# Kernel optimization log

Measured on AMD Instinct MI355X. Metric: run time of the kernel, lower is better.

Reference implementation:

```python
import jax, jax.numpy as jnp
from jax import lax
import numpy as np


def _conv(x, w):
    # x: [B,Cin,H,W], w: [Cout,Cin,kh,kw] -> [B,Cout,H,W], SAME padding
    return lax.conv_general_dilated(x, w, (1, 1), 'SAME')


def setup_inputs() -> dict:
    key = jax.random.key(0)
    ks = jax.random.split(key, 16)
    B, Hh, W = 8, 256, 256
    inputs = jax.random.normal(ks[0], (B, Hh, W), jnp.float32)
    H0 = jax.random.normal(ks[1], (B, Hh, W), jnp.float32)
    C0 = jax.random.normal(ks[2], (B, 2, Hh, W), jnp.float32)
    # learned scalars: c2 ~ U(0,1), sf ~ N(0, 0.01) shifted away from 0 (it is a divisor)
    c2 = jax.random.uniform(ks[3], (1,), jnp.float32, 0.0, 1.0)
    sf = 0.01 * jax.random.normal(ks[4], (1,), jnp.float32) + 0.02
    # RedNet (assumed small conv encoder-decoder): 1->32->64->32->1, 3x3 SAME, ReLU
    w1 = 0.1 * jax.random.normal(ks[5], (32, 1, 3, 3), jnp.float32)
    b1 = jnp.zeros((32,), jnp.float32)
    w2 = 0.1 * jax.random.normal(ks[6], (64, 32, 3, 3), jnp.float32)
    b2 = jnp.zeros((64,), jnp.float32)
    w3 = 0.1 * jax.random.normal(ks[7], (32, 64, 3, 3), jnp.float32)
    b3 = jnp.zeros((32,), jnp.float32)
    w4 = 0.1 * jax.random.normal(ks[8], (1, 32, 3, 3), jnp.float32)
    b4 = jnp.zeros((1,), jnp.float32)
    return dict(inputs=inputs, H0=H0, C0=C0, c2=c2, sf=sf,
                w1=w1, b1=b1, w2=w2, b2=b2, w3=w3, b3=b3, w4=w4, b4=b4)


def reference(inputs, H0, C0, c2, sf, w1, b1, w2, b2, w3, b3, w4, b4):
    # Fixed 5-point Laplacian stencil (non-trainable in the original module)
    lap_k = jnp.array([[0., 1., 0.], [1., -4., 1.], [0., 1., 0.]],
                      dtype=inputs.dtype)[None, None]  # [1,1,3,3]

    # torch chain: C' = permute/matmul(Wcc^T)/permute + wcu*U
    #   reduces exactly to: C'[:,0] = inputs, C'[:,1] = C_old[:,0]
    C_new = jnp.stack([inputs, C0[:, 0]], axis=1)  # [B,2,H,W]

    V = inputs - H0  # [B,H,W]

    # H = whc . C' = 2*C'[:,0] - C'[:,1] = 2*inputs - C_old[:,0]
    lap = _conv(inputs[:, None], lap_k)[:, 0]  # [B,H,W]
    H = 2.0 * inputs - C0[:, 0] + c2 * lap

    # RedNet on scaled residual V
    h = (V / sf)[:, None]  # [B,1,H,W]
    h = jax.nn.relu(_conv(h, w1) + b1[None, :, None, None])
    h = jax.nn.relu(_conv(h, w2) + b2[None, :, None, None])
    h = jax.nn.relu(_conv(h, w3) + b3[None, :, None, None])
    V_hat = (_conv(h, w4) + b4[None, :, None, None])[:, 0] * sf  # [B,H,W]

    outputs = H + V_hat
    return (outputs, H, C_new, V, V_hat)
```

## Files before the change

kernel.cpp:

```cpp
#include <hip/hip_runtime.h>

#define PLANE 65536
#define WIDTH 256
#define PADW 258
#define PADPLANE 66564

typedef __bf16 v8bf __attribute__((ext_vector_type(8)));
typedef float  v4f  __attribute__((ext_vector_type(4)));

typedef const __attribute__((address_space(1))) unsigned int* gas_ptr;
typedef __attribute__((address_space(3))) unsigned int* las_ptr;

__device__ __forceinline__ void gl_lds(const void* g, void* l) {
  __builtin_amdgcn_global_load_lds((gas_ptr)g, (las_ptr)l, 16, 0, 0);
}

__device__ __forceinline__ int swz(int c) {
  return (c & ~7) | ((c & 7) ^ ((c >> 3) & 7));
}

__device__ __forceinline__ unsigned int pack2(float a, float b) {
  __bf16 ba = (__bf16)a, bb = (__bf16)b;
  unsigned short sa = __builtin_bit_cast(unsigned short, ba);
  unsigned short sb = __builtin_bit_cast(unsigned short, bb);
  return (unsigned int)sa | ((unsigned int)sb << 16);
}

__global__ __launch_bounds__(256) void prep_k(
    const float* __restrict__ inputs, const float* __restrict__ H0,
    const float* __restrict__ C0, const float* __restrict__ c2p,
    const float* __restrict__ sfp, float* __restrict__ dout,
    float* __restrict__ vs)
{
  int p = blockIdx.x * 256 + threadIdx.x;
  int b = p >> 16;
  int i = p & 65535;
  int y = i >> 8;
  int x = i & 255;
  float in   = inputs[p];
  float h0   = H0[p];
  float c0a  = C0[b * 131072 + i];
  float up    = (y > 0)   ? inputs[p - 256] : 0.f;
  float down  = (y < 255) ? inputs[p + 256] : 0.f;
  float left  = (x > 0)   ? inputs[p - 1]   : 0.f;
  float right = (x < 255) ? inputs[p + 1]   : 0.f;
  float lap = up + down + left + right - 4.f * in;
  float c2 = c2p[0];
  float sf = sfp[0];
  float Hv = 2.f * in - c0a + c2 * lap;
  float V  = in - h0;
  dout[524288 + p]  = Hv;
  dout[2097152 + p] = V;
  dout[1048576 + b * 131072 + i]         = in;
  dout[1048576 + b * 131072 + 65536 + i] = c0a;
  vs[p] = V / sf;
}

__global__ __launch_bounds__(256) void wtrans_k(
    const float* __restrict__ w1, const float* __restrict__ w2,
    const float* __restrict__ w3, const float* __restrict__ w4,
    float* __restrict__ w1t, __bf16* __restrict__ B2t,
    __bf16* __restrict__ B3t, float* __restrict__ w4t)
{
  int t = blockIdx.x * 256 + threadIdx.x;
  if (t < 288) {
    int tap = t >> 5, cout = t & 31;
    w1t[t] = w1[cout * 9 + tap];
  }
  int t2 = t - 288;
  if (t2 >= 0 && t2 < 18432) {
    int cout = t2 / 288, k = t2 % 288;
    int tap = k / 32, cin = k % 32;
    B2t[t2] = (__bf16)w2[cout * 288 + cin * 9 + tap];
  }
  int t3 = t - (288 + 18432);
  if (t3 >= 0 && t3 < 18432) {
    int cout = t3 / 576, k = t3 % 576;
    int tap = k / 64, cin = k % 64;
    B3t[t3] = (__bf16)w3[cout * 576 + cin * 9 + tap];
  }
  int t4 = t - (288 + 18432 + 18432);
  if (t4 >= 0 && t4 < 288) {
    int tap = t4 >> 5, cin = t4 & 31;
    w4t[t4] = w4[cin * 9 + tap];
  }
}

#define R1 (8 * 1028 * 16)
#define R2 (8 * 1028 * 32)
#define R3 (8 * 1028 * 16)
__global__ __launch_bounds__(256) void zero_k(
    __bf16* __restrict__ a1, __bf16* __restrict__ a2, __bf16* __restrict__ a3)
{
  int t = blockIdx.x * 256 + threadIdx.x;
  unsigned int* p; int C2, idx;
  if (t < R1)            { p = (unsigned int*)a1; C2 = 16; idx = t; }
  else if (t < R1 + R2)  { p = (unsigned int*)a2; C2 = 32; idx = t - R1; }
  else if (t < R1+R2+R3) { p = (unsigned int*)a3; C2 = 16; idx = t - R1 - R2; }
  else return;
  int ch = idx % C2;
  int pr = idx / C2;
  int b = pr / 1028, r = pr % 1028;
  int y, x;
  if      (r < 258) { y = 0;           x = r; }
  else if (r < 516) { y = 257;         x = r - 258; }
  else if (r < 772) { y = r - 516 + 1; x = 0; }
  else              { y = r - 772 + 1; x = 257; }
  p[((size_t)b * PADPLANE + y * PADW + x) * C2 + ch] = 0;
}

__global__ __launch_bounds__(256) void conv1_k(
    const float* __restrict__ vs, const float* __restrict__ w1t,
    const float* __restrict__ b1, __bf16* __restrict__ act1)
{
  int x = threadIdx.x, y = blockIdx.x, b = blockIdx.y;
  const float* ip = vs + ((size_t)b << 16) + y * WIDTH + x;
  float acc[32];
  #pragma unroll
  for (int i = 0; i < 32; i++) acc[i] = b1[i];
  #pragma unroll
  for (int tap = 0; tap < 9; tap++) {
    int dy = tap / 3 - 1, dx = tap % 3 - 1;
    int yy = y + dy, xx = x + dx;
    bool ok = (yy >= 0 && yy < 256 && xx >= 0 && xx < 256);
    float v = ok ? ip[dy * WIDTH + dx] : 0.f;
    const float* wp = w1t + tap * 32;
    #pragma unroll
    for (int i = 0; i < 32; i++) acc[i] = fmaf(wp[i], v, acc[i]);
  }
  unsigned int u[16];
  #pragma unroll
  for (int j = 0; j < 16; j++)
    u[j] = pack2(fmaxf(acc[2*j], 0.f), fmaxf(acc[2*j+1], 0.f));
  size_t pa = ((size_t)b * PADPLANE + (y+1) * PADW + (x+1)) * 32;
  uint4* op = reinterpret_cast<uint4*>(act1 + pa);
  #pragma unroll
  for (int j = 0; j < 4; j++)
    op[j] = make_uint4(u[4*j], u[4*j+1], u[4*j+2], u[4*j+3]);
}

#define C2ROWB 8320
template<int ROWS>
__global__ __launch_bounds__(256, 2) void conv2_k(
    const __bf16* __restrict__ in, const __bf16* __restrict__ Bt,
    const float* __restrict__ bias, __bf16* __restrict__ out)
{
  const int lane = threadIdx.x & 63, wave = threadIdx.x >> 6;
  const int l15 = lane & 15, q = lane >> 4;
  const int y0 = blockIdx.x * ROWS, xt = blockIdx.y, b = blockIdx.z;
  const int x0 = xt * 128;
  __shared__ __align__(16) char smem[3 * C2ROWB];
  const __bf16* plane = in + (size_t)b * PADPLANE * 32;

  auto stage = [&](int pr, char* lrow) {
    const char* g = (const char*)(plane + ((size_t)pr * PADW + x0) * 32);
    const int base = wave * 130;
    #pragma unroll
    for (int j = 0; j < 2; j++) {
      int c = base + j * 64 + lane;
      gl_lds(g + (size_t)swz(c) * 16, lrow + (base + j * 64) * 16);
    }
    if (lane < 2) {
      int c = base + 128 + lane;
      gl_lds(g + (size_t)swz(c) * 16, lrow + (base + 128) * 16);
    }
  };

  v8bf breg[9][4];
  #pragma unroll
  for (int tap = 0; tap < 9; tap++)
    #pragma unroll
    for (int nt = 0; nt < 4; nt++)
      breg[tap][nt] = *(const v8bf*)(Bt + (size_t)(nt * 16 + l15) * 288
                                        + tap * 32 + q * 8);
  float bv[4];
  #pragma unroll
  for (int nt = 0; nt < 4; nt++) bv[nt] = bias[nt * 16 + l15];

  #pragma unroll
  for (int r = 0; r < 3; r++) stage(y0 + r, smem + r * C2ROWB);
  __syncthreads();

  for (int i = 0; i < ROWS; i++) {
    v4f acc[2][4];
    #pragma unroll
    for (int mt = 0; mt < 2; mt++)
      #pragma unroll
      for (int nt = 0; nt < 4; nt++)
        acc[mt][nt] = (v4f){bv[nt], bv[nt], bv[nt], bv[nt]};

    #pragma unroll
    for (int tap = 0; tap < 9; tap++) {
      const int dy = tap / 3, dx = tap % 3;
      const char* srow = smem + ((i + dy) % 3) * C2ROWB;
      v8bf af[2];
      #pragma unroll
      for (int mt = 0; mt < 2; mt++) {
        int P = wave * 32 + mt * 16 + l15 + dx;
        af[mt] = *(const v8bf*)(srow + (size_t)swz(P * 4 + q) * 16);
      }
      #pragma unroll
      for (int mt = 0; mt < 2; mt++)
        #pragma unroll
        for (int nt = 0; nt < 4; nt++)
          acc[mt][nt] = __builtin_amdgcn_mfma_f32_16x16x32_bf16(
              af[mt], breg[tap][nt], acc[mt][nt], 0, 0, 0);
    }
    {
      size_t rb = ((size_t)b * PADPLANE + (size_t)(y0 + i + 1) * PADW
                   + x0 + 1) * 64;
      #pragma unroll
      for (int mt = 0; mt < 2; mt++) {
        #pragma unroll
        for (int r = 0; r < 4; r++) {
          size_t pa = rb + (size_t)(wave * 32 + mt * 16 + q * 4 + r) * 64;
          #pragma unroll
          for (int nt = 0; nt < 4; nt++)
            out[pa + nt * 16 + l15] = (__bf16)fmaxf(acc[mt][nt][r], 0.f);
        }
      }
    }
    __syncthreads();
    if (i + 3 < ROWS + 2)
      stage(y0 + i + 3, smem + (i % 3) * C2ROWB);
    __syncthreads();
  }
}

#define C3ROWB 16640
template<int ROWS>
__global__ __launch_bounds__(256, 2) void conv3_k(
    const __bf16* __restrict__ in, const __bf16* __restrict__ Bt,
    const float* __restrict__ bias, __bf16* __restrict__ out)
{
  const int lane = threadIdx.x & 63, wave = threadIdx.x >> 6;
  const int l15 = lane & 15, q = lane >> 4;
  const int y0 = blockIdx.x * ROWS, xt = blockIdx.y, b = blockIdx.z;
  const int x0 = xt * 128;
  __shared__ __align__(16) char smem[4 * C3ROWB];
  const __bf16* plane = in + (size_t)b * PADPLANE * 64;

  auto stage = [&](int pr, char* lrow) {
    const char* g = (const char*)(plane + ((size_t)pr * PADW + x0) * 64);
    const int base = wave * 260;
    #pragma unroll
    for (int j = 0; j < 4; j++) {
      int c = base + j * 64 + lane;
      gl_lds(g + (size_t)swz(c) * 16, lrow + (base + j * 64) * 16);
    }
    if (lane < 4) {
      int c = base + 256 + lane;
      gl_lds(g + (size_t)swz(c) * 16, lrow + (base + 256) * 16);
    }
  };

  v8bf breg[9][2][2];
  #pragma unroll
  for (int tap = 0; tap < 9; tap++)
    #pragma unroll
    for (int kb = 0; kb < 2; kb++)
      #pragma unroll
      for (int nt = 0; nt < 2; nt++)
        breg[tap][kb][nt] = *(const v8bf*)(Bt + (size_t)(nt * 16 + l15) * 576
                                              + tap * 64 + kb * 32 + q * 8);
  float bv[2] = {bias[l15], bias[16 + l15]};

  #pragma unroll
  for (int r = 0; r < 4; r++) stage(y0 + r, smem + r * C3ROWB);
  __syncthreads();

  for (int ps = 0; ps < ROWS / 2; ps++) {
    v4f acc[2][2][2];
    #pragma unroll
    for (int rr = 0; rr < 2; rr++)
      #pragma unroll
      for (int mt = 0; mt < 2; mt++)
        #pragma unroll
        for (int nt = 0; nt < 2; nt++)
          acc[rr][mt][nt] = (v4f){bv[nt], bv[nt], bv[nt], bv[nt]};

    #pragma unroll
    for (int t = 0; t < 4; t++) {
      const char* srow = smem + ((2 * ps + t) & 3) * C3ROWB;
      #pragma unroll
      for (int dx = 0; dx < 3; dx++) {
        #pragma unroll
        for (int kb = 0; kb < 2; kb++) {
          v8bf af[2];
          #pragma unroll
          for (int mt = 0; mt < 2; mt++) {
            int P = wave * 32 + mt * 16 + l15 + dx;
            af[mt] = *(const v8bf*)(srow + (size_t)swz(P * 8 + kb * 4 + q) * 16);
          }
          #pragma unroll
          for (int mt = 0; mt < 2; mt++)
            #pragma unroll
            for (int nt = 0; nt < 2; nt++) {
              if (t <= 2)
                acc[0][mt][nt] = __builtin_amdgcn_mfma_f32_16x16x32_bf16(
                    af[mt], breg[t * 3 + dx][kb][nt], acc[0][mt][nt], 0, 0, 0);
              if (t >= 1)
                acc[1][mt][nt] = __builtin_amdgcn_mfma_f32_16x16x32_bf16(
                    af[mt], breg[(t - 1) * 3 + dx][kb][nt], acc[1][mt][nt],
                    0, 0, 0);
            }
        }
      }
    }
    {
      #pragma unroll
      for (int rr = 0; rr < 2; rr++) {
        size_t rb = ((size_t)b * PADPLANE
                     + (size_t)(y0 + 2 * ps + rr + 1) * PADW + x0 + 1) * 32;
        #pragma unroll
        for (int mt = 0; mt < 2; mt++) {
          #pragma unroll
          for (int r = 0; r < 4; r++) {
            size_t pa = rb + (size_t)(wave * 32 + mt * 16 + q * 4 + r) * 32;
            #pragma unroll
            for (int nt = 0; nt < 2; nt++)
              out[pa + nt * 16 + l15] = (__bf16)fmaxf(acc[rr][mt][nt][r], 0.f);
          }
        }
      }
    }
    __syncthreads();
    if (ps + 1 < ROWS / 2) {
      stage(y0 + 2 * ps + 4, smem + ((2 * ps) & 3) * C3ROWB);
      stage(y0 + 2 * ps + 5, smem + ((2 * ps + 1) & 3) * C3ROWB);
    }
    __syncthreads();
  }
}

#define C4ROWS 4
__global__ __launch_bounds__(256) void conv4_k(
    const __bf16* __restrict__ act3, const float* __restrict__ w4t,
    const float* __restrict__ b4, const float* __restrict__ sfp,
    float* __restrict__ dout)
{
  const int x = threadIdx.x, y0 = blockIdx.x * C4ROWS, b = blockIdx.y;
  const float b4v = b4[0], sf = sfp[0];
  const uint4* base = (const uint4*)(act3 + (size_t)b * PADPLANE * 32);
  float accs[3] = {b4v, b4v, b4v};

  #pragma unroll
  for (int t = 0; t < C4ROWS + 2; t++) {
    const int pr = y0 + t;
    const uint4* rp = base + ((size_t)pr * PADW + x) * 4;
    uint4 L[12];
    #pragma unroll
    for (int j = 0; j < 12; j++) L[j] = rp[j];
    #pragma unroll
    for (int j = 0; j < 12; j++) {
      const int dx = j >> 2, c0 = (j & 3) * 8;
      unsigned int uu[4] = {L[j].x, L[j].y, L[j].z, L[j].w};
      float f[8];
      #pragma unroll
      for (int k = 0; k < 4; k++) {
        f[2*k]   = __builtin_bit_cast(float, uu[k] << 16);
        f[2*k+1] = __builtin_bit_cast(float, uu[k] & 0xFFFF0000u);
      }
      #pragma unroll
      for (int dyp = 0; dyp < 3; dyp++) {
        if (dyp <= t && t - dyp < C4ROWS) {
          const int slot = (t - dyp) % 3;
          const float* wp = w4t + (dyp * 3 + dx) * 32 + c0;
          #pragma unroll
          for (int k = 0; k < 8; k++)
            accs[slot] = fmaf(wp[k], f[k], accs[slot]);
        }
      }
    }
    if (t >= 2) {
      const int r = y0 + t - 2, slot = (t - 2) % 3;
      size_t p0 = ((size_t)b << 16) + (size_t)r * WIDTH + x;
      float vh = accs[slot] * sf;
      dout[p0]           = dout[524288 + p0] + vh;
      dout[2621440 + p0] = vh;
      accs[slot] = b4v;
    }
  }
}

extern "C" void kernel_launch(void* const* d_in, const int* in_sizes, int n_in,
                              void* d_out, int out_size, void* d_ws, size_t ws_size,
                              hipStream_t stream) {
  const float* inputs = (const float*)d_in[0];
  const float* H0     = (const float*)d_in[1];
  const float* C0     = (const float*)d_in[2];
  const float* c2     = (const float*)d_in[3];
  const float* sf     = (const float*)d_in[4];
  const float* w1     = (const float*)d_in[5];
  const float* b1     = (const float*)d_in[6];
  const float* w2     = (const float*)d_in[7];
  const float* b2     = (const float*)d_in[8];
  const float* w3     = (const float*)d_in[9];
  const float* b3     = (const float*)d_in[10];
  const float* w4     = (const float*)d_in[11];
  const float* b4     = (const float*)d_in[12];
  float* out = (float*)d_out;
  float* ws  = (float*)d_ws;

  float*  vs   = ws;
  float*  w1t  = ws + 524288;
  float*  w4t  = ws + 524576;
  __bf16* B2t  = (__bf16*)(ws + 524864);
  __bf16* B3t  = (__bf16*)(ws + 534080);
  __bf16* act1 = (__bf16*)(ws + 543296);
  __bf16* act2 = act1 + (size_t)8 * PADPLANE * 32;
  __bf16* act3 = act2 + (size_t)8 * PADPLANE * 64;

  prep_k<<<2048, 256, 0, stream>>>(inputs, H0, C0, c2, sf, out, vs);
  wtrans_k<<<147, 256, 0, stream>>>(w1, w2, w3, w4, w1t, B2t, B3t, w4t);
  zero_k<<<2056, 256, 0, stream>>>(act1, act2, act3);
  conv1_k<<<dim3(256, 8), 256, 0, stream>>>(vs, w1t, b1, act1);
  conv2_k<8><<<dim3(32, 2, 8), 256, 0, stream>>>(act1, B2t, b2, act2);
  conv3_k<8><<<dim3(32, 2, 8), 256, 0, stream>>>(act2, B3t, b3, act3);
  conv4_k<<<dim3(64, 8), 256, 0, stream>>>(act3, w4t, b4, sf, out);
}
```

Before: 187.8 us.

## Fuse prep into conv1 and merge weight transform with halo zeroing

The elementwise prep kernel is folded into conv1. Each thread now loads its 3x3 neighbourhood of inputs and H0, computes V/sf on the fly for the conv taps, and writes H, V and C_new directly, so the intermediate vs buffer is no longer written and re-read. The weight transpose and padding-zero kernels are merged into a single launch, cutting the launch count from seven to five. The cost is redundant neighbourhood loads of inputs and H0 (mostly cache hits) and a division replaced by multiplication with a reciprocal, which can change rounding slightly.

```diff
diff --git a/kernel.cpp b/kernel.cpp
--- a/kernel.cpp
+++ b/kernel.cpp
@@ -26,78 +26,48 @@
   return (unsigned int)sa | ((unsigned int)sb << 16);
 }
 
-__global__ __launch_bounds__(256) void prep_k(
-    const float* __restrict__ inputs, const float* __restrict__ H0,
-    const float* __restrict__ C0, const float* __restrict__ c2p,
-    const float* __restrict__ sfp, float* __restrict__ dout,
-    float* __restrict__ vs)
-{
-  int p = blockIdx.x * 256 + threadIdx.x;
-  int b = p >> 16;
-  int i = p & 65535;
-  int y = i >> 8;
-  int x = i & 255;
-  float in   = inputs[p];
-  float h0   = H0[p];
-  float c0a  = C0[b * 131072 + i];
-  float up    = (y > 0)   ? inputs[p - 256] : 0.f;
-  float down  = (y < 255) ? inputs[p + 256] : 0.f;
-  float left  = (x > 0)   ? inputs[p - 1]   : 0.f;
-  float right = (x < 255) ? inputs[p + 1]   : 0.f;
-  float lap = up + down + left + right - 4.f * in;
-  float c2 = c2p[0];
-  float sf = sfp[0];
-  float Hv = 2.f * in - c0a + c2 * lap;
-  float V  = in - h0;
-  dout[524288 + p]  = Hv;
-  dout[2097152 + p] = V;
-  dout[1048576 + b * 131072 + i]         = in;
-  dout[1048576 + b * 131072 + 65536 + i] = c0a;
-  vs[p] = V / sf;
-}
-
-__global__ __launch_bounds__(256) void wtrans_k(
+#define WT_N 37440
+#define ZR_N (8 * 1028 * 64)
+__global__ __launch_bounds__(256) void wz_k(
     const float* __restrict__ w1, const float* __restrict__ w2,
     const float* __restrict__ w3, const float* __restrict__ w4,
     float* __restrict__ w1t, __bf16* __restrict__ B2t,
-    __bf16* __restrict__ B3t, float* __restrict__ w4t)
+    __bf16* __restrict__ B3t, float* __restrict__ w4t,
+    __bf16* __restrict__ a1, __bf16* __restrict__ a2,
+    __bf16* __restrict__ a3)
 {
   int t = blockIdx.x * 256 + threadIdx.x;
-  if (t < 288) {
-    int tap = t >> 5, cout = t & 31;
-    w1t[t] = w1[cout * 9 + tap];
-  }
-  int t2 = t - 288;
-  if (t2 >= 0 && t2 < 18432) {
-    int cout = t2 / 288, k = t2 % 288;
-    int tap = k / 32, cin = k % 32;
-    B2t[t2] = (__bf16)w2[cout * 288 + cin * 9 + tap];
-  }
-  int t3 = t - (288 + 18432);
-  if (t3 >= 0 && t3 < 18432) {
-    int cout = t3 / 576, k = t3 % 576;
-    int tap = k / 64, cin = k % 64;
-    B3t[t3] = (__bf16)w3[cout * 576 + cin * 9 + tap];
-  }
-  int t4 = t - (288 + 18432 + 18432);
-  if (t4 >= 0 && t4 < 288) {
-    int tap = t4 >> 5, cin = t4 & 31;
-    w4t[t4] = w4[cin * 9 + tap];
-  }
-}
-
-#define R1 (8 * 1028 * 16)
-#define R2 (8 * 1028 * 32)
-#define R3 (8 * 1028 * 16)
-__global__ __launch_bounds__(256) void zero_k(
-    __bf16* __restrict__ a1, __bf16* __restrict__ a2, __bf16* __restrict__ a3)
-{
-  int t = blockIdx.x * 256 + threadIdx.x;
-  unsigned int* p; int C2, idx;
-  if (t < R1)            { p = (unsigned int*)a1; C2 = 16; idx = t; }
-  else if (t < R1 + R2)  { p = (unsigned int*)a2; C2 = 32; idx = t - R1; }
-  else if (t < R1+R2+R3) { p = (unsigned int*)a3; C2 = 16; idx = t - R1 - R2; }
-  else return;
+  if (t < WT_N) {
+    if (t < 288) {
+      int tap = t >> 5, cout = t & 31;
+      w1t[t] = w1[cout * 9 + tap];
+    }
+    int t2 = t - 288;
+    if (t2 >= 0 && t2 < 18432) {
+      int cout = t2 / 288, k = t2 % 288;
+      int tap = k / 32, cin = k % 32;
+      B2t[t2] = (__bf16)w2[cout * 288 + cin * 9 + tap];
+    }
+    int t3 = t - (288 + 18432);
+    if (t3 >= 0 && t3 < 18432) {
+      int cout = t3 / 576, k = t3 % 576;
+      int tap = k / 64, cin = k % 64;
+      B3t[t3] = (__bf16)w3[cout * 576 + cin * 9 + tap];
+    }
+    int t4 = t - (288 + 18432 + 18432);
+    if (t4 >= 0 && t4 < 288) {
+      int tap = t4 >> 5, cin = t4 & 31;
+      w4t[t4] = w4[cin * 9 + tap];
+    }
+    return;
+  }
+  int idx = t - WT_N;
+  if (idx >= ZR_N) return;
+  unsigned int* p; int C2;
+  const int R1 = 8 * 1028 * 16, R2 = 8 * 1028 * 32;
+  if (idx < R1)           { p = (unsigned int*)a1; C2 = 16; }
+  else if (idx < R1 + R2) { p = (unsigned int*)a2; C2 = 32; idx -= R1; }
+  else                    { p = (unsigned int*)a3; C2 = 16; idx -= R1 + R2; }
   int ch = idx % C2;
   int pr = idx / C2;
   int b = pr / 1028, r = pr % 1028;
@@ -109,21 +79,46 @@
   p[((size_t)b * PADPLANE + y * PADW + x) * C2 + ch] = 0;
 }
 
-__global__ __launch_bounds__(256) void conv1_k(
-    const float* __restrict__ vs, const float* __restrict__ w1t,
-    const float* __restrict__ b1, __bf16* __restrict__ act1)
+__global__ __launch_bounds__(256) void prepconv1_k(
+    const float* __restrict__ inputs, const float* __restrict__ H0,
+    const float* __restrict__ C0, const float* __restrict__ c2p,
+    const float* __restrict__ sfp, const float* __restrict__ w1t,
+    const float* __restrict__ b1, float* __restrict__ dout,
+    __bf16* __restrict__ act1)
 {
-  int x = threadIdx.x, y = blockIdx.x, b = blockIdx.y;
-  const float* ip = vs + ((size_t)b << 16) + y * WIDTH + x;
+  const int x = threadIdx.x, y = blockIdx.x, b = blockIdx.y;
+  const int p = b * PLANE + y * WIDTH + x;
+  const float c2 = c2p[0], sf = sfp[0], rsf = 1.0f / sf;
+
+  float iv[3][3], hv[3][3];
+  #pragma unroll
+  for (int dy = 0; dy < 3; dy++) {
+    int yy = y + dy - 1;
+    #pragma unroll
+    for (int dx = 0; dx < 3; dx++) {
+      int xx = x + dx - 1;
+      bool ok = (yy >= 0 && yy < 256 && xx >= 0 && xx < 256);
+      int pn = p + (dy - 1) * WIDTH + (dx - 1);
+      iv[dy][dx] = ok ? inputs[pn] : 0.f;
+      hv[dy][dx] = ok ? H0[pn]     : 0.f;
+    }
+  }
+  const float in = iv[1][1], h0 = hv[1][1];
+  const float c0a = C0[b * 131072 + y * WIDTH + x];
+  float lap = iv[0][1] + iv[2][1] + iv[1][0] + iv[1][2] - 4.f * in;
+  float Hv = 2.f * in - c0a + c2 * lap;
+  float V  = in - h0;
+  dout[524288 + p]  = Hv;
+  dout[2097152 + p] = V;
+  dout[1048576 + b * 131072 + y * WIDTH + x]         = in;
+  dout[1048576 + b * 131072 + 65536 + y * WIDTH + x] = c0a;
+
   float acc[32];
   #pragma unroll
   for (int i = 0; i < 32; i++) acc[i] = b1[i];
   #pragma unroll
   for (int tap = 0; tap < 9; tap++) {
-    int dy = tap / 3 - 1, dx = tap % 3 - 1;
-    int yy = y + dy, xx = x + dx;
-    bool ok = (yy >= 0 && yy < 256 && xx >= 0 && xx < 256);
-    float v = ok ? ip[dy * WIDTH + dx] : 0.f;
+    float v = (iv[tap / 3][tap % 3] - hv[tap / 3][tap % 3]) * rsf;
     const float* wp = w1t + tap * 32;
     #pragma unroll
     for (int i = 0; i < 32; i++) acc[i] = fmaf(wp[i], v, acc[i]);
@@ -402,19 +397,18 @@
   float* out = (float*)d_out;
   float* ws  = (float*)d_ws;
 
-  float*  vs   = ws;
-  float*  w1t  = ws + 524288;
-  float*  w4t  = ws + 524576;
-  __bf16* B2t  = (__bf16*)(ws + 524864);
-  __bf16* B3t  = (__bf16*)(ws + 534080);
-  __bf16* act1 = (__bf16*)(ws + 543296);
+  float*  w1t  = ws;
+  float*  w4t  = ws + 288;
+  __bf16* B2t  = (__bf16*)(ws + 576);
+  __bf16* B3t  = (__bf16*)(ws + 9792);
+  __bf16* act1 = (__bf16*)(ws + 19008);
   __bf16* act2 = act1 + (size_t)8 * PADPLANE * 32;
   __bf16* act3 = act2 + (size_t)8 * PADPLANE * 64;
 
-  prep_k<<<2048, 256, 0, stream>>>(inputs, H0, C0, c2, sf, out, vs);
-  wtrans_k<<<147, 256, 0, stream>>>(w1, w2, w3, w4, w1t, B2t, B3t, w4t);
-  zero_k<<<2056, 256, 0, stream>>>(act1, act2, act3);
-  conv1_k<<<dim3(256, 8), 256, 0, stream>>>(vs, w1t, b1, act1);
+  wz_k<<<2203, 256, 0, stream>>>(w1, w2, w3, w4, w1t, B2t, B3t, w4t,
+                                 act1, act2, act3);
+  prepconv1_k<<<dim3(256, 8), 256, 0, stream>>>(inputs, H0, C0, c2, sf,
+                                                w1t, b1, out, act1);
   conv2_k<8><<<dim3(32, 2, 8), 256, 0, stream>>>(act1, B2t, b2, act2);
   conv3_k<8><<<dim3(32, 2, 8), 256, 0, stream>>>(act2, B3t, b3, act3);
   conv4_k<<<dim3(64, 8), 256, 0, stream>>>(act3, w4t, b4, sf, out);
```

Result: faster. 181.0 us (-3.6%).
